# Kernel tuning notes

Measured on AMD Instinct MI355X. Metric: run time of the kernel, lower is better.

The kernel has to match this reference:

```python
import jax, jax.numpy as jnp
import numpy as np

B, N, P, D, H = 16, 256, 8, 512, 8
E = P * D  # 4096, flattened patch embedding width


def _sincos_pos_embed(q_len, d_model):
    # PatchTST-style 'sincos' positional encoding (learn_pe=False buffer)
    pe = np.zeros((q_len, d_model), dtype=np.float64)
    position = np.arange(q_len, dtype=np.float64)[:, None]
    div_term = np.exp(np.arange(0, d_model, 2, dtype=np.float64) * -(np.log(10000.0) / d_model))
    pe[:, 0::2] = np.sin(position * div_term)
    pe[:, 1::2] = np.cos(position * div_term)
    pe = pe - pe.mean()
    pe = pe / (pe.std() * 10)
    return jnp.asarray(pe, dtype=jnp.float32)


def setup_inputs() -> dict:
    key = jax.random.key(0)
    ks = jax.random.split(key, 10)
    s = 0.02
    return {
        "x": jax.random.normal(ks[0], (B, N, P, D), dtype=jnp.float32),
        "pos_embed": _sincos_pos_embed(N, E),
        "W_embed": jax.random.normal(ks[1], (E, E), dtype=jnp.float32) * s,
        "b_embed": jnp.zeros((E,), dtype=jnp.float32),
        "Wq": jax.random.normal(ks[2], (E, E), dtype=jnp.float32) * s,
        "bq": jnp.zeros((E,), dtype=jnp.float32),
        "Wk": jax.random.normal(ks[3], (E, E), dtype=jnp.float32) * s,
        "bk": jnp.zeros((E,), dtype=jnp.float32),
        "Wv": jax.random.normal(ks[4], (E, E), dtype=jnp.float32) * s,
        "bv": jnp.zeros((E,), dtype=jnp.float32),
        "Wo": jax.random.normal(ks[5], (E, E), dtype=jnp.float32) * s,
        "bo": jnp.zeros((E,), dtype=jnp.float32),
    }


def reference(x, pos_embed, W_embed, b_embed, Wq, bq, Wk, bk, Wv, bv, Wo, bo):
    b, n, p, d = x.shape
    h = H
    dh = E // h  # per-head dim = patch_size * d_keys
    xe = x.reshape(b, n, p * d)                       # B N (P D)
    xe = xe @ W_embed.T + b_embed                     # embed_linear
    xe = xe + pos_embed                               # pos embed (dropout=0, eval)
    q = (xe @ Wq.T + bq).reshape(b, n, h, dh)
    k = (xe @ Wk.T + bk).reshape(b, n, h, dh)
    v = (xe @ Wv.T + bv).reshape(b, n, h, dh)
    scale = 1.0 / np.sqrt(d // h)                     # NOTE: uses d_model//H, not E//H (faithful)
    attn_scores = jnp.einsum('bnhd,bmhd->bhnm', q, k) * scale
    attn_weights = jax.nn.softmax(attn_scores, axis=-1)
    out = jnp.einsum('bhnm,bmhd->bnhd', attn_weights, v).reshape(b, n, h * dh)
    out = out @ Wo.T + bo
    out = out.reshape(b, n, p, d)
    return out, attn_weights
```

## Files before the change

### kernel.cpp

```cpp
#include <hip/hip_runtime.h>
#include <hip/hip_bf16.h>


typedef unsigned short u16;
typedef _Float16 f16;
typedef __attribute__((ext_vector_type(8))) _Float16 v8h;
typedef __attribute__((ext_vector_type(8))) short vu16x8;
typedef __attribute__((ext_vector_type(4))) float vf32x4;

#define MFMA_F16(a, b, c) __builtin_amdgcn_mfma_f32_16x16x32_f16(a, b, c, 0, 0, 0)

__device__ __forceinline__ void gld16(const void* g, void* l) {
    __builtin_amdgcn_global_load_lds((const __attribute__((address_space(1))) void*)g,
                                     (__attribute__((address_space(3))) void*)l,
                                     16, 0, 0);
}

__global__ __launch_bounds__(256) void tof16(const float* __restrict__ s,
                                             f16* __restrict__ d) {
    const size_t i = ((size_t)blockIdx.x * 256 + threadIdx.x) * 4;
    const float4 v = *(const float4*)(s + i);
    d[i + 0] = (f16)v.x; d[i + 1] = (f16)v.y;
    d[i + 2] = (f16)v.z; d[i + 3] = (f16)v.w;
}

template <int MODE>
__global__ __launch_bounds__(512, 2)
void gemm8_nt(const f16* __restrict__ A, const f16* __restrict__ Bw,
              const float* __restrict__ bias, const float* __restrict__ pos,
              f16* __restrict__ Ch, float* __restrict__ Cf) {
    __shared__ __align__(16) u16 sA[2][16384];
    __shared__ __align__(16) u16 sB[2][16384];
    const int t = threadIdx.x;
    const int lane = t & 63, w = t >> 6;
    const int wm = w >> 2, wn = w & 3;
    const int l15 = lane & 15, lg = lane >> 4;
    const int wg = ((blockIdx.x & 7) << 5) + (blockIdx.x >> 3);
    const int m0 = (wg >> 4) << 8, n0 = (wg & 15) << 8;

    int srow[4], scol[4];
#pragma unroll
    for (int i = 0; i < 4; ++i) {
        const int c = t + (i << 9);
        srow[i] = c >> 3;
        scol[i] = (((c & 7) ^ (srow[i] & 7)) << 3);
    }
    const int rA = (wm << 7) + l15;
    const int rB = (wn << 6) + l15;
    const int xA = rA & 7, xB = rB & 7;

    vf32x4 acc[8][4] = {};

#define STAGE(buf, k0) do {                                                    \
    _Pragma("unroll")                                                          \
    for (int i = 0; i < 4; ++i) {                                              \
        const int c = t + (i << 9);                                            \
        gld16(A  + (((size_t)(m0 + srow[i])) << 12) + (k0) + scol[i],          \
              &sA[buf][c * 8]);                                                \
    }                                                                          \
    _Pragma("unroll")                                                          \
    for (int i = 0; i < 4; ++i) {                                              \
        const int c = t + (i << 9);                                            \
        gld16(Bw + (((size_t)(n0 + srow[i])) << 12) + (k0) + scol[i],          \
              &sB[buf][c * 8]);                                                \
    }                                                                          \
} while (0)

    STAGE(0, 0);

    for (int kt = 0; kt < 64; ++kt) {
        const int cb = kt & 1;
        if (kt < 63) {
            STAGE(cb ^ 1, (kt + 1) << 6);
            asm volatile("s_waitcnt vmcnt(8)" ::: "memory");
        } else {
            asm volatile("s_waitcnt vmcnt(0)" ::: "memory");
        }
        __builtin_amdgcn_s_barrier();
        asm volatile("" ::: "memory");
#pragma unroll
        for (int kk = 0; kk < 2; ++kk) {
            const int ccA = (((kk << 2) + lg) ^ xA) << 3;
            const int ccB = (((kk << 2) + lg) ^ xB) << 3;
            v8h av[8], bv[4];
#pragma unroll
            for (int m = 0; m < 8; ++m)
                av[m] = *(const v8h*)(&sA[cb][(rA << 6) + (m << 10) + ccA]);
#pragma unroll
            for (int n = 0; n < 4; ++n)
                bv[n] = *(const v8h*)(&sB[cb][(rB << 6) + (n << 10) + ccB]);
            asm volatile("s_waitcnt lgkmcnt(0)" ::: "memory");
            __builtin_amdgcn_sched_barrier(0);
            __builtin_amdgcn_s_setprio(1);
#pragma unroll
            for (int m = 0; m < 8; ++m)
#pragma unroll
                for (int n = 0; n < 4; ++n)
                    acc[m][n] = MFMA_F16(av[m], bv[n], acc[m][n]);
            __builtin_amdgcn_s_setprio(0);
        }
        __builtin_amdgcn_s_barrier();
        asm volatile("" ::: "memory");
    }
#undef STAGE

#pragma unroll
    for (int n = 0; n < 4; ++n) {
        const int col = n0 + (wn << 6) + (n << 4) + l15;
        const float bvv = bias[col];
#pragma unroll
        for (int m = 0; m < 8; ++m) {
#pragma unroll
            for (int r = 0; r < 4; ++r) {
                const int row = m0 + (wm << 7) + (m << 4) + (lg << 2) + r;
                float v = acc[m][n][r] + bvv;
                if (MODE == 0) v += pos[((size_t)(row & 255) << 12) + col];
                if (MODE == 2)
                    Cf[((size_t)row << 12) + col] = v;
                else
                    Ch[((size_t)row << 12) + col] = (f16)v;
            }
        }
    }
}

__global__ __launch_bounds__(256)
void attn_scores(const f16* __restrict__ q, const f16* __restrict__ k,
                 float* __restrict__ Pf, f16* __restrict__ Pb) {
    const int blk = blockIdx.x;
    const int bh = blk >> 2, it = blk & 3;
    const int b = bh >> 3, h = bh & 7;
    const size_t qoff = ((size_t)(b * 256 + it * 64) << 12) + (h << 9);
    const size_t koff = ((size_t)(b * 256) << 12) + (h << 9);
    __shared__ __align__(16) u16 Qs[64 * 64];
    __shared__ __align__(16) u16 Ks[256 * 64];
    __shared__ float red[4][64];

    const int t = threadIdx.x;
    const int lane = t & 63, w = t >> 6;
    const int l15 = lane & 15, lg = lane >> 4;

    vf32x4 acc[4][4] = {};

    for (int k0 = 0; k0 < 512; k0 += 64) {
#pragma unroll
        for (int i = 0; i < 2; ++i) {
            const int c = t + (i << 8);
            const int row = c >> 3, c8 = (c & 7) << 3;
            gld16(q + qoff + ((size_t)row << 12) + k0 + c8, Qs + c * 8);
        }
#pragma unroll
        for (int i = 0; i < 8; ++i) {
            const int c = t + (i << 8);
            const int row = c >> 3, c8 = (c & 7) << 3;
            gld16(k + koff + ((size_t)row << 12) + k0 + c8, Ks + c * 8);
        }
        __syncthreads();
#pragma unroll
        for (int kk = 0; kk < 2; ++kk) {
            v8h af[4], bf[4];
#pragma unroll
            for (int m = 0; m < 4; ++m)
                af[m] = *(const v8h*)(Qs + (m * 16 + l15) * 64 + kk * 32 + lg * 8);
#pragma unroll
            for (int n = 0; n < 4; ++n)
                bf[n] = *(const v8h*)(Ks + (w * 64 + n * 16 + l15) * 64 + kk * 32 + lg * 8);
#pragma unroll
            for (int m = 0; m < 4; ++m)
#pragma unroll
                for (int n = 0; n < 4; ++n)
                    acc[m][n] = MFMA_F16(af[m], bf[n], acc[m][n]);
        }
        __syncthreads();
    }

#pragma unroll
    for (int m = 0; m < 4; ++m)
#pragma unroll
        for (int n = 0; n < 4; ++n) acc[m][n] *= 0.125f;

    float gm[4][4];
#pragma unroll
    for (int m = 0; m < 4; ++m)
#pragma unroll
        for (int r = 0; r < 4; ++r) {
            float v = fmaxf(fmaxf(acc[m][0][r], acc[m][1][r]),
                            fmaxf(acc[m][2][r], acc[m][3][r]));
#pragma unroll
            for (int off = 1; off < 16; off <<= 1) v = fmaxf(v, __shfl_xor(v, off));
            gm[m][r] = v;
        }
    if (l15 == 0) {
#pragma unroll
        for (int m = 0; m < 4; ++m)
#pragma unroll
            for (int r = 0; r < 4; ++r) red[w][m * 16 + lg * 4 + r] = gm[m][r];
    }
    __syncthreads();
#pragma unroll
    for (int m = 0; m < 4; ++m)
#pragma unroll
        for (int r = 0; r < 4; ++r) {
            const int row = m * 16 + lg * 4 + r;
            gm[m][r] = fmaxf(fmaxf(red[0][row], red[1][row]),
                             fmaxf(red[2][row], red[3][row]));
        }
    __syncthreads();

    float gs[4][4];
#pragma unroll
    for (int m = 0; m < 4; ++m)
#pragma unroll
        for (int r = 0; r < 4; ++r) {
            float s = 0.f;
#pragma unroll
            for (int n = 0; n < 4; ++n) {
                const float e = __expf(acc[m][n][r] - gm[m][r]);
                acc[m][n][r] = e;
                s += e;
            }
#pragma unroll
            for (int off = 1; off < 16; off <<= 1) s += __shfl_xor(s, off);
            gs[m][r] = s;
        }
    if (l15 == 0) {
#pragma unroll
        for (int m = 0; m < 4; ++m)
#pragma unroll
            for (int r = 0; r < 4; ++r) red[w][m * 16 + lg * 4 + r] = gs[m][r];
    }
    __syncthreads();

    const size_t pbase = ((size_t)bh * 256 + it * 64) * 256;
#pragma unroll
    for (int m = 0; m < 4; ++m)
#pragma unroll
        for (int r = 0; r < 4; ++r) {
            const int row = m * 16 + lg * 4 + r;
            const float inv = 1.0f / (red[0][row] + red[1][row] +
                                      red[2][row] + red[3][row]);
#pragma unroll
            for (int n = 0; n < 4; ++n) {
                const int col = w * 64 + n * 16 + l15;
                const float p = acc[m][n][r] * inv;
                Pf[pbase + (size_t)row * 256 + col] = p;
                Pb[pbase + (size_t)row * 256 + col] = (f16)p;
            }
        }
}

__global__ __launch_bounds__(256)
void attn_pv(const f16* __restrict__ P, const f16* __restrict__ V,
             f16* __restrict__ O) {
    __shared__ __align__(16) u16 Ps[128 * 64];
    __shared__ __align__(16) u16 Vt[128 * 72];
    const int t = threadIdx.x;
    const int lane = t & 63, w = t >> 6;
    const int wr = (w >> 1) << 6, wc = (w & 1) << 6;
    const int l15 = lane & 15, lg = lane >> 4;
    const int blk = blockIdx.x;
    const int bh = blk >> 3, mt = (blk >> 2) & 1, nt = blk & 3;
    const int b = bh >> 3, h = bh & 7;
    const f16* Pbp = P + ((size_t)bh << 16) + ((size_t)mt << 15);
    const u16* Vb = (const u16*)V + ((size_t)(b * 256) << 12) + (h << 9) + (nt << 7);

    vf32x4 acc[4][4] = {};

    for (int k0 = 0; k0 < 256; k0 += 64) {
#pragma unroll
        for (int i = 0; i < 4; ++i) {
            const int c = t + (i << 8);
            const int row = c >> 3, c8 = (c & 7) << 3;
            gld16(Pbp + (size_t)row * 256 + k0 + c8, Ps + c * 8);
        }
#pragma unroll
        for (int pp = 0; pp < 4; ++pp) {
            const int kr = pp * 16 + (t >> 4);
            const int c8 = (t & 15) << 3;
            vu16x8 vv = *(const vu16x8*)(Vb + ((size_t)(k0 + kr) << 12) + c8);
#pragma unroll
            for (int c = 0; c < 8; ++c) Vt[(c8 + c) * 72 + kr] = (u16)vv[c];
        }
        __syncthreads();
#pragma unroll
        for (int kk = 0; kk < 2; ++kk) {
            v8h af[4], bf[4];
#pragma unroll
            for (int m = 0; m < 4; ++m)
                af[m] = *(const v8h*)(Ps + (wr + m * 16 + l15) * 64 + kk * 32 + lg * 8);
#pragma unroll
            for (int n = 0; n < 4; ++n)
                bf[n] = *(const v8h*)(Vt + (wc + n * 16 + l15) * 72 + kk * 32 + lg * 8);
#pragma unroll
            for (int m = 0; m < 4; ++m)
#pragma unroll
                for (int n = 0; n < 4; ++n)
                    acc[m][n] = MFMA_F16(af[m], bf[n], acc[m][n]);
        }
        __syncthreads();
    }

#pragma unroll
    for (int m = 0; m < 4; ++m)
#pragma unroll
        for (int n = 0; n < 4; ++n) {
            const int col = (h << 9) + (nt << 7) + wc + n * 16 + l15;
#pragma unroll
            for (int r = 0; r < 4; ++r) {
                const int row = b * 256 + mt * 128 + wr + m * 16 + lg * 4 + r;
                O[((size_t)row << 12) + col] = (f16)acc[m][n][r];
            }
        }
}

extern "C" void kernel_launch(void* const* d_in, const int* in_sizes, int n_in,
                              void* d_out, int out_size, void* d_ws, size_t ws_size,
                              hipStream_t stream) {
    const float* x   = (const float*)d_in[0];
    const float* pos = (const float*)d_in[1];
    const float* wE  = (const float*)d_in[2];
    const float* bE  = (const float*)d_in[3];
    const float* wQ  = (const float*)d_in[4];
    const float* bq  = (const float*)d_in[5];
    const float* wK  = (const float*)d_in[6];
    const float* bk  = (const float*)d_in[7];
    const float* wV  = (const float*)d_in[8];
    const float* bv  = (const float*)d_in[9];
    const float* wO  = (const float*)d_in[10];
    const float* bo  = (const float*)d_in[11];

    float* out  = (float*)d_out;
    float* Pout = out + (size_t)16777216;

    char* W = (char*)d_ws;
    const size_t MB = 1024 * 1024;
    f16* xf    = (f16*)(W + 0 * MB);
    f16* wslab = (f16*)(W + 32 * MB);
    f16* xe    = (f16*)(W + 64 * MB);
    f16* qs    = (f16*)(W + 96 * MB);
    f16* ks    = (f16*)(W + 128 * MB);
    f16* vs    = (f16*)(W + 160 * MB);
    f16* Pb    = (f16*)(W + 192 * MB);
    f16* ao    = xf;

    const int CVG = 16384;

    tof16<<<CVG, 256, 0, stream>>>(x, xf);
    tof16<<<CVG, 256, 0, stream>>>(wE, wslab);
    gemm8_nt<0><<<256, 512, 0, stream>>>(xf, wslab, bE, pos, xe, nullptr);

    tof16<<<CVG, 256, 0, stream>>>(wQ, wslab);
    gemm8_nt<1><<<256, 512, 0, stream>>>(xe, wslab, bq, nullptr, qs, nullptr);

    tof16<<<CVG, 256, 0, stream>>>(wK, wslab);
    gemm8_nt<1><<<256, 512, 0, stream>>>(xe, wslab, bk, nullptr, ks, nullptr);

    tof16<<<CVG, 256, 0, stream>>>(wV, wslab);
    gemm8_nt<1><<<256, 512, 0, stream>>>(xe, wslab, bv, nullptr, vs, nullptr);

    attn_scores<<<512, 256, 0, stream>>>(qs, ks, Pout, Pb);
    attn_pv<<<1024, 256, 0, stream>>>(Pb, vs, ao);

    tof16<<<CVG, 256, 0, stream>>>(wO, wslab);
    gemm8_nt<2><<<256, 512, 0, stream>>>(ao, wslab, bo, nullptr, nullptr, out);
}
```

Before: 866.9 us.

## Merge fp16 conversions into one launch and interleave LDS reads with MFMAs

Six separate fp32-to-fp16 conversion launches become one 2D-grid kernel, with each weight written to its own workspace slab. Q and the fp16 attention probabilities are placed in unused parts of the output buffer to make room. Inside the GEMM main loop, the two k-substeps are split into four quarter-blocks with partial lgkmcnt waits, so LDS fragment loads overlap MFMA execution instead of waiting for all loads first. This cuts launch overhead and LDS latency stalls, at the cost of more workspace and tighter register pressure from the extra fragment buffers.

```diff
diff --git a/kernel.cpp b/kernel.cpp
--- a/kernel.cpp
+++ b/kernel.cpp
@@ -16,12 +16,14 @@
                                      16, 0, 0);
 }
 
-__global__ __launch_bounds__(256) void tof16(const float* __restrict__ s,
-                                             f16* __restrict__ d) {
+struct Cv6 { const float* s[6]; f16* d[6]; };
+
+__global__ __launch_bounds__(256) void convert6(Cv6 p) {
+    const int a = blockIdx.y;
     const size_t i = ((size_t)blockIdx.x * 256 + threadIdx.x) * 4;
-    const float4 v = *(const float4*)(s + i);
-    d[i + 0] = (f16)v.x; d[i + 1] = (f16)v.y;
-    d[i + 2] = (f16)v.z; d[i + 3] = (f16)v.w;
+    const float4 v = *(const float4*)(p.s[a] + i);
+    f16* d = p.d[a] + i;
+    d[0] = (f16)v.x; d[1] = (f16)v.y; d[2] = (f16)v.z; d[3] = (f16)v.w;
 }
 
 template <int MODE>
@@ -48,6 +50,10 @@
     const int rA = (wm << 7) + l15;
     const int rB = (wn << 6) + l15;
     const int xA = rA & 7, xB = rB & 7;
+    const int ccA0 = ((0 + lg) ^ xA) << 3;
+    const int ccA1 = ((4 + lg) ^ xA) << 3;
+    const int ccB0 = ((0 + lg) ^ xB) << 3;
+    const int ccB1 = ((4 + lg) ^ xB) << 3;
 
     vf32x4 acc[8][4] = {};
 
@@ -77,30 +83,66 @@
             asm volatile("s_waitcnt vmcnt(0)" ::: "memory");
         }
         __builtin_amdgcn_s_barrier();
-        asm volatile("" ::: "memory");
-#pragma unroll
-        for (int kk = 0; kk < 2; ++kk) {
-            const int ccA = (((kk << 2) + lg) ^ xA) << 3;
-            const int ccB = (((kk << 2) + lg) ^ xB) << 3;
-            v8h av[8], bv[4];
-#pragma unroll
-            for (int m = 0; m < 8; ++m)
-                av[m] = *(const v8h*)(&sA[cb][(rA << 6) + (m << 10) + ccA]);
-#pragma unroll
-            for (int n = 0; n < 4; ++n)
-                bv[n] = *(const v8h*)(&sB[cb][(rB << 6) + (n << 10) + ccB]);
-            asm volatile("s_waitcnt lgkmcnt(0)" ::: "memory");
-            __builtin_amdgcn_sched_barrier(0);
-            __builtin_amdgcn_s_setprio(1);
-#pragma unroll
-            for (int m = 0; m < 8; ++m)
-#pragma unroll
-                for (int n = 0; n < 4; ++n)
-                    acc[m][n] = MFMA_F16(av[m], bv[n], acc[m][n]);
-            __builtin_amdgcn_s_setprio(0);
-        }
+
+        v8h b0[4], b1[4], a0[4], a1[4], a2[4], a3[4];
+#pragma unroll
+        for (int n = 0; n < 4; ++n)
+            b0[n] = *(const v8h*)(&sB[cb][(rB << 6) + (n << 10) + ccB0]);
+#pragma unroll
+        for (int m = 0; m < 4; ++m)
+            a0[m] = *(const v8h*)(&sA[cb][(rA << 6) + (m << 10) + ccA0]);
+        __builtin_amdgcn_sched_barrier(0);
+#pragma unroll
+        for (int m = 0; m < 4; ++m)
+            a1[m] = *(const v8h*)(&sA[cb][(rA << 6) + ((m + 4) << 10) + ccA0]);
+        asm volatile("s_waitcnt lgkmcnt(4)" ::: "memory");
+        __builtin_amdgcn_sched_barrier(0);
+        __builtin_amdgcn_s_setprio(1);
+#pragma unroll
+        for (int m = 0; m < 4; ++m)
+#pragma unroll
+            for (int n = 0; n < 4; ++n)
+                acc[m][n] = MFMA_F16(a0[m], b0[n], acc[m][n]);
+        __builtin_amdgcn_s_setprio(0);
+        __builtin_amdgcn_sched_barrier(0);
+#pragma unroll
+        for (int n = 0; n < 4; ++n)
+            b1[n] = *(const v8h*)(&sB[cb][(rB << 6) + (n << 10) + ccB1]);
+#pragma unroll
+        for (int m = 0; m < 4; ++m)
+            a2[m] = *(const v8h*)(&sA[cb][(rA << 6) + (m << 10) + ccA1]);
+        asm volatile("s_waitcnt lgkmcnt(8)" ::: "memory");
+        __builtin_amdgcn_sched_barrier(0);
+        __builtin_amdgcn_s_setprio(1);
+#pragma unroll
+        for (int m = 0; m < 4; ++m)
+#pragma unroll
+            for (int n = 0; n < 4; ++n)
+                acc[m + 4][n] = MFMA_F16(a1[m], b0[n], acc[m + 4][n]);
+        __builtin_amdgcn_s_setprio(0);
+        __builtin_amdgcn_sched_barrier(0);
+#pragma unroll
+        for (int m = 0; m < 4; ++m)
+            a3[m] = *(const v8h*)(&sA[cb][(rA << 6) + ((m + 4) << 10) + ccA1]);
+        asm volatile("s_waitcnt lgkmcnt(4)" ::: "memory");
+        __builtin_amdgcn_sched_barrier(0);
+        __builtin_amdgcn_s_setprio(1);
+#pragma unroll
+        for (int m = 0; m < 4; ++m)
+#pragma unroll
+            for (int n = 0; n < 4; ++n)
+                acc[m][n] = MFMA_F16(a2[m], b1[n], acc[m][n]);
+        __builtin_amdgcn_s_setprio(0);
+        asm volatile("s_waitcnt lgkmcnt(0)" ::: "memory");
+        __builtin_amdgcn_sched_barrier(0);
+        __builtin_amdgcn_s_setprio(1);
+#pragma unroll
+        for (int m = 0; m < 4; ++m)
+#pragma unroll
+            for (int n = 0; n < 4; ++n)
+                acc[m + 4][n] = MFMA_F16(a3[m], b1[n], acc[m + 4][n]);
+        __builtin_amdgcn_s_setprio(0);
         __builtin_amdgcn_s_barrier();
-        asm volatile("" ::: "memory");
     }
 #undef STAGE
 
@@ -334,33 +376,35 @@
 
     char* W = (char*)d_ws;
     const size_t MB = 1024 * 1024;
-    f16* xf    = (f16*)(W + 0 * MB);
-    f16* wslab = (f16*)(W + 32 * MB);
-    f16* xe    = (f16*)(W + 64 * MB);
-    f16* qs    = (f16*)(W + 96 * MB);
-    f16* ks    = (f16*)(W + 128 * MB);
-    f16* vs    = (f16*)(W + 160 * MB);
-    f16* Pb    = (f16*)(W + 192 * MB);
-    f16* ao    = xf;
-
-    const int CVG = 16384;
-
-    tof16<<<CVG, 256, 0, stream>>>(x, xf);
-    tof16<<<CVG, 256, 0, stream>>>(wE, wslab);
-    gemm8_nt<0><<<256, 512, 0, stream>>>(xf, wslab, bE, pos, xe, nullptr);
-
-    tof16<<<CVG, 256, 0, stream>>>(wQ, wslab);
-    gemm8_nt<1><<<256, 512, 0, stream>>>(xe, wslab, bq, nullptr, qs, nullptr);
-
-    tof16<<<CVG, 256, 0, stream>>>(wK, wslab);
-    gemm8_nt<1><<<256, 512, 0, stream>>>(xe, wslab, bk, nullptr, ks, nullptr);
-
-    tof16<<<CVG, 256, 0, stream>>>(wV, wslab);
-    gemm8_nt<1><<<256, 512, 0, stream>>>(xe, wslab, bv, nullptr, vs, nullptr);
+    f16* xf  = (f16*)(W + 0 * MB);
+    f16* xe  = (f16*)(W + 32 * MB);
+    f16* ks  = (f16*)(W + 64 * MB);
+    f16* vs  = (f16*)(W + 96 * MB);
+    f16* wEs = (f16*)(W + 128 * MB);
+    f16* wQs = (f16*)(W + 160 * MB);
+    f16* wKs = (f16*)(W + 192 * MB);
+    f16* wVs = (f16*)(W + 224 * MB);
+    f16* wOs = (f16*)(W + 256 * MB);
+    f16* ao  = xf;
+    f16* qs  = (f16*)out;
+    f16* Pb  = (f16*)(out + (size_t)8388608);
+
+    Cv6 cv;
+    cv.s[0] = x;  cv.d[0] = xf;
+    cv.s[1] = wE; cv.d[1] = wEs;
+    cv.s[2] = wQ; cv.d[2] = wQs;
+    cv.s[3] = wK; cv.d[3] = wKs;
+    cv.s[4] = wV; cv.d[4] = wVs;
+    cv.s[5] = wO; cv.d[5] = wOs;
+    convert6<<<dim3(16384, 6), 256, 0, stream>>>(cv);
+
+    gemm8_nt<0><<<256, 512, 0, stream>>>(xf, wEs, bE, pos, xe, nullptr);
+    gemm8_nt<1><<<256, 512, 0, stream>>>(xe, wQs, bq, nullptr, qs, nullptr);
+    gemm8_nt<1><<<256, 512, 0, stream>>>(xe, wKs, bk, nullptr, ks, nullptr);
+    gemm8_nt<1><<<256, 512, 0, stream>>>(xe, wVs, bv, nullptr, vs, nullptr);
 
     attn_scores<<<512, 256, 0, stream>>>(qs, ks, Pout, Pb);
     attn_pv<<<1024, 256, 0, stream>>>(Pb, vs, ao);
 
-    tof16<<<CVG, 256, 0, stream>>>(wO, wslab);
-    gemm8_nt<2><<<256, 512, 0, stream>>>(ao, wslab, bo, nullptr, nullptr, out);
-}
+    gemm8_nt<2><<<256, 512, 0, stream>>>(ao, wOs, bo, nullptr, nullptr, out);
+}
```

Measured after the change: 919.9 us. 6.1% more time.
